# Optimization experiments

Measured on AMD Instinct MI355X. Metric: run time of the kernel, lower is better.

Reference implementation:

```python
import jax, jax.numpy as jnp
import numpy as np

B, N, D, H, F = 2, 2048, 512, 8, 8
HD = D // H

def setup_inputs() -> dict:
    key = jax.random.key(0)
    ks = jax.random.split(key, 11)
    s = 1.0 / np.sqrt(D)
    return {
        "x": jax.random.normal(ks[0], (B, N, D), dtype=jnp.float32),
        "phase_coords": jax.random.uniform(ks[1], (B, N, F), dtype=jnp.float32) * 6.28,
        "Wq": jax.random.normal(ks[2], (D, D), dtype=jnp.float32) * s,
        "bq": jax.random.normal(ks[3], (D,), dtype=jnp.float32) * 0.01,
        "Wk": jax.random.normal(ks[4], (D, D), dtype=jnp.float32) * s,
        "bk": jax.random.normal(ks[5], (D,), dtype=jnp.float32) * 0.01,
        "Wv": jax.random.normal(ks[6], (D, D), dtype=jnp.float32) * s,
        "bv": jax.random.normal(ks[7], (D,), dtype=jnp.float32) * 0.01,
        "Wo": jax.random.normal(ks[8], (D, D), dtype=jnp.float32) * s,
        "bo": jax.random.normal(ks[9], (D,), dtype=jnp.float32) * 0.01,
        "phase_bias": jax.random.normal(ks[10], (H, F), dtype=jnp.float32) * 0.1,
    }

def reference(x, phase_coords, Wq, bq, Wk, bk, Wv, bv, Wo, bo, phase_bias):
    b, n, _ = x.shape
    def proj(W, bias):
        # [B,N,D] -> [B,H,N,HD]
        return (x @ W.T + bias).reshape(b, n, H, HD).transpose(0, 2, 1, 3)
    Q, K, V = proj(Wq, bq), proj(Wk, bk), proj(Wv, bv)
    scores = jnp.einsum("bhqd,bhkd->bhqk", Q, K) / np.sqrt(HD)
    # phase coherence bias: cos of pairwise phase diffs, weighted per head
    phase_diff = phase_coords[:, :, None, :] - phase_coords[:, None, :, :]  # [B,N,N,F]
    coherence = jnp.cos(phase_diff)
    bias = jnp.einsum("bqkf,hf->bhqk", coherence, phase_bias)
    scores = scores + bias
    attn = jax.nn.softmax(scores, axis=-1)
    attended = jnp.einsum("bhqk,bhkd->bhqd", attn, V)
    attended = attended.transpose(0, 2, 1, 3).reshape(b, n, D)
    return attended @ Wo.T + bo
```

## Files before the change

### kernel.cpp

```cpp
#include <hip/hip_runtime.h>
#include <stdint.h>

typedef unsigned short u16;
typedef unsigned int   u32;
typedef __bf16 bf16x8 __attribute__((ext_vector_type(8)));
typedef float  f32x4  __attribute__((ext_vector_type(4)));
typedef u16    u16x8  __attribute__((ext_vector_type(8)));
typedef u16    u16x4  __attribute__((ext_vector_type(4)));

#define B_  2
#define N_  2048
#define D_  512
#define H_  8
#define HD_ 64

__device__ __forceinline__ u16 f2bf(float f) {
  union { float f; u32 u; } v; v.f = f;
  u32 r = v.u + 0x7FFFu + ((v.u >> 16) & 1u);
  return (u16)(r >> 16);
}
__device__ __forceinline__ float bf2f(u16 s) {
  union { u32 u; float f; } v; v.u = ((u32)s) << 16; return v.f;
}

__device__ __forceinline__ void gload_lds16(const void* g, void* l) {
  __builtin_amdgcn_global_load_lds(
      (const __attribute__((address_space(1))) void*)g,
      (__attribute__((address_space(3))) void*)l, 16, 0, 0);
}

__global__ __launch_bounds__(256) void k_prep(
    const float* __restrict__ x, const float* __restrict__ pc,
    const float* __restrict__ Wq, const float* __restrict__ bq,
    const float* __restrict__ Wk, const float* __restrict__ bk,
    const float* __restrict__ Wv, const float* __restrict__ bv,
    const float* __restrict__ Wo,
    u16* __restrict__ xb, u16* __restrict__ wqkvb, float* __restrict__ bqkv,
    u16* __restrict__ wob, u16* __restrict__ pcs)
{
  int gid = blockIdx.x * blockDim.x + threadIdx.x;
  int stride = gridDim.x * blockDim.x;
  for (int i = gid; i < B_ * N_ * D_; i += stride) xb[i] = f2bf(x[i]);
  for (int i = gid; i < 3 * D_ * D_; i += stride) {
    int r = i >> 9;
    float v;
    if (r < 512)       v = Wq[i] * 0.125f;
    else if (r < 1024) v = Wk[i - 512 * 512];
    else               v = Wv[i - 1024 * 512];
    wqkvb[i] = f2bf(v);
  }
  for (int i = gid; i < 3 * D_; i += stride) {
    float v;
    if (i < 512)       v = bq[i] * 0.125f;
    else if (i < 1024) v = bk[i - 512];
    else               v = bv[i - 1024];
    bqkv[i] = v;
  }
  for (int i = gid; i < D_ * D_; i += stride) wob[i] = f2bf(Wo[i]);
  for (int i = gid; i < B_ * N_; i += stride) {
#pragma unroll
    for (int f = 0; f < 8; f++) {
      float a = pc[i * 8 + f];
      pcs[i * 16 + f]     = f2bf(__cosf(a));
      pcs[i * 16 + 8 + f] = f2bf(__sinf(a));
    }
  }
}

template <int MODE>
__global__ __launch_bounds__(256) void k_gemm(
    const u16* __restrict__ A, const u16* __restrict__ Bm,
    const float* __restrict__ bias,
    u16* __restrict__ Qp, u16* __restrict__ Kp, u16* __restrict__ Vt,
    float* __restrict__ Of)
{
  __shared__ u16 As[2][64 * 64];
  __shared__ u16 Bs[2][128 * 64];
  const int tid = threadIdx.x;
  const int wave = tid >> 6, lane = tid & 63;
  const int fr = lane & 15, kg = lane >> 4;
  const int m0 = blockIdx.x * 64, n0 = blockIdx.y * 128;
  const int wr = (wave >> 1) * 32, wc = (wave & 1) * 64;

  f32x4 acc[2][4];
#pragma unroll
  for (int i = 0; i < 2; i++)
#pragma unroll
    for (int j = 0; j < 4; j++)
#pragma unroll
      for (int r = 0; r < 4; r++) acc[i][j][r] = 0.f;

  auto stage = [&](int buf, int k0) {
#pragma unroll
    for (int u = 0; u < 2; u++) {
      int chunk = (wave * 2 + u) * 64 + lane;
      int row = chunk >> 3, cl = chunk & 7;
      gload_lds16(A + (size_t)(m0 + row) * 512 + k0 + ((cl ^ (row & 7)) << 3),
                  &As[buf][(wave * 2 + u) * 512]);
    }
#pragma unroll
    for (int u = 0; u < 4; u++) {
      int chunk = (wave * 4 + u) * 64 + lane;
      int row = chunk >> 3, cl = chunk & 7;
      gload_lds16(Bm + (size_t)(n0 + row) * 512 + k0 + ((cl ^ (row & 7)) << 3),
                  &Bs[buf][(wave * 4 + u) * 512]);
    }
  };

  stage(0, 0);
  asm volatile("s_waitcnt vmcnt(0)" ::: "memory");
  __syncthreads();

#pragma unroll
  for (int s = 0; s < 8; s++) {
    const int cb = s & 1;
    if (s < 7) stage(cb ^ 1, (s + 1) * 64);
#pragma unroll
    for (int ksub = 0; ksub < 2; ksub++) {
      bf16x8 af[2], bf[4];
#pragma unroll
      for (int i = 0; i < 2; i++)
        af[i] = *(const bf16x8*)&As[cb][(wr + i * 16 + fr) * 64 + (((ksub * 4 + kg) ^ (fr & 7)) << 3)];
#pragma unroll
      for (int j = 0; j < 4; j++)
        bf[j] = *(const bf16x8*)&Bs[cb][(wc + j * 16 + fr) * 64 + (((ksub * 4 + kg) ^ (fr & 7)) << 3)];
#pragma unroll
      for (int i = 0; i < 2; i++)
#pragma unroll
        for (int j = 0; j < 4; j++)
          acc[i][j] = __builtin_amdgcn_mfma_f32_16x16x32_bf16(af[i], bf[j], acc[i][j], 0, 0, 0);
    }
    asm volatile("s_waitcnt vmcnt(0)" ::: "memory");
    __syncthreads();
  }

  if (MODE == 1) {
#pragma unroll
    for (int j = 0; j < 4; j++) {
      int col = n0 + wc + j * 16 + fr;
      float bc = bias[col];
#pragma unroll
      for (int i = 0; i < 2; i++)
#pragma unroll
        for (int r = 0; r < 4; r++)
          Of[(size_t)(m0 + wr + i * 16 + kg * 4 + r) * 512 + col] = acc[i][j][r] + bc;
  } } else {
    const int seg = n0 >> 9;
    const int nb = n0 & 511;
    if (seg < 2) {
      u16* dst = seg ? Kp : Qp;
#pragma unroll
      for (int j = 0; j < 4; j++) {
        int col = nb + wc + j * 16 + fr;
        float bc = bias[n0 + wc + j * 16 + fr];
#pragma unroll
        for (int i = 0; i < 2; i++)
#pragma unroll
          for (int r = 0; r < 4; r++)
            dst[(size_t)(m0 + wr + i * 16 + kg * 4 + r) * 512 + col] = f2bf(acc[i][j][r] + bc);
      }
    } else {
#pragma unroll
      for (int j = 0; j < 4; j++) {
        int cc = nb + wc + j * 16 + fr;
        float bc = bias[n0 + wc + j * 16 + fr];
        int h = cc >> 6, d = cc & 63;
#pragma unroll
        for (int i = 0; i < 2; i++) {
          int row = m0 + wr + i * 16 + kg * 4;
          int b = row >> 11, n = row & 2047;
          u16x4 o;
#pragma unroll
          for (int r = 0; r < 4; r++) o[r] = f2bf(acc[i][j][r] + bc);
          *(u16x4*)&Vt[((size_t)(b * 8 + h) * 64 + d) * N_ + n] = o;
        }
      }
    }
  }
}

__global__ __launch_bounds__(256) void k_attn(
    const u16* __restrict__ Qp, const u16* __restrict__ Kp,
    const u16* __restrict__ Vt, const u16* __restrict__ pcs,
    const float* __restrict__ pb, u16* __restrict__ att)
{
  const int bh = blockIdx.y, b = bh >> 3, h = bh & 7;
  const int q0 = blockIdx.x * 64;
  const int tid = threadIdx.x, wave = tid >> 6, lane = tid & 63;
  const int fr = lane & 15, kg = lane >> 4;

  __shared__ u16 Klds[2][64 * 72];
  __shared__ u16 Kext[2][64 * 40];
  __shared__ u16 Vlds[2][64 * 72];
  __shared__ u16 Plds[4][16 * 72];

  for (int i = tid; i < 2 * 64 * 16; i += 256) {
    int bb = i >> 10, rr = (i >> 4) & 63, c = 16 + (i & 15);
    Kext[bb][rr * 40 + c] = 0;
  }

  const int r0 = tid >> 3, c0 = (tid & 7) * 8;
  const int r1 = 32 + r0;
  const int er = tid >> 1, ec = (tid & 1) * 8;

  bf16x8 qa[3];
  {
    int gq = b * N_ + q0 + wave * 16 + fr;
#pragma unroll
    for (int ks = 0; ks < 2; ks++)
      qa[ks] = *(const bf16x8*)&Qp[(size_t)gq * D_ + h * HD_ + ks * 32 + kg * 8];
    union { bf16x8 v; u16 s[8]; } qe;
    if (kg < 2) {
      u16x8 cs = *(const u16x8*)&pcs[(size_t)gq * 16 + kg * 8];
#pragma unroll
      for (int j = 0; j < 8; j++) qe.s[j] = f2bf(pb[h * 8 + j] * bf2f(cs[j]));
    } else {
#pragma unroll
      for (int j = 0; j < 8; j++) qe.s[j] = 0;
    }
    qa[2] = qe.v;
  }

  f32x4 accO[4];
#pragma unroll
  for (int d = 0; d < 4; d++)
#pragma unroll
    for (int r = 0; r < 4; r++) accO[d][r] = 0.f;
  float Lacc[4] = {0.f, 0.f, 0.f, 0.f};

  {
    u16x8 k0v = *(const u16x8*)&Kp[(size_t)(b * N_ + r0) * D_ + h * HD_ + c0];
    u16x8 k1v = *(const u16x8*)&Kp[(size_t)(b * N_ + r1) * D_ + h * HD_ + c0];
    u16x8 v0v = *(const u16x8*)&Vt[((size_t)bh * HD_ + r0) * N_ + c0];
    u16x8 v1v = *(const u16x8*)&Vt[((size_t)bh * HD_ + r1) * N_ + c0];
    *(u16x8*)&Klds[0][r0 * 72 + c0] = k0v;
    *(u16x8*)&Klds[0][r1 * 72 + c0] = k1v;
    *(u16x8*)&Vlds[0][r0 * 72 + c0] = v0v;
    *(u16x8*)&Vlds[0][r1 * 72 + c0] = v1v;
    if (tid < 128) {
      u16x8 ev = *(const u16x8*)&pcs[(size_t)(b * N_ + er) * 16 + ec];
      *(u16x8*)&Kext[0][er * 40 + ec] = ev;
    }
  }
  __syncthreads();

  for (int t = 0; t < 32; t++) {
    const int cb = t & 1;
    const bool pf = (t < 31);
    u16x8 kreg0, kreg1, vreg0, vreg1, ereg;
    if (pf) {
      int nk = (t + 1) * 64;
      kreg0 = *(const u16x8*)&Kp[(size_t)(b * N_ + nk + r0) * D_ + h * HD_ + c0];
      kreg1 = *(const u16x8*)&Kp[(size_t)(b * N_ + nk + r1) * D_ + h * HD_ + c0];
      vreg0 = *(const u16x8*)&Vt[((size_t)bh * HD_ + r0) * N_ + nk + c0];
      vreg1 = *(const u16x8*)&Vt[((size_t)bh * HD_ + r1) * N_ + nk + c0];
      if (tid < 128) ereg = *(const u16x8*)&pcs[(size_t)(b * N_ + nk + er) * 16 + ec];
    }

    f32x4 accS[4];
#pragma unroll
    for (int j = 0; j < 4; j++)
#pragma unroll
      for (int r = 0; r < 4; r++) accS[j][r] = 0.f;
#pragma unroll
    for (int ks = 0; ks < 2; ks++) {
#pragma unroll
      for (int j = 0; j < 4; j++) {
        bf16x8 kb = *(const bf16x8*)&Klds[cb][(j * 16 + fr) * 72 + ks * 32 + kg * 8];
        accS[j] = __builtin_amdgcn_mfma_f32_16x16x32_bf16(qa[ks], kb, accS[j], 0, 0, 0);
      }
    }
#pragma unroll
    for (int j = 0; j < 4; j++) {
      bf16x8 kb = *(const bf16x8*)&Kext[cb][(j * 16 + fr) * 40 + kg * 8];
      accS[j] = __builtin_amdgcn_mfma_f32_16x16x32_bf16(qa[2], kb, accS[j], 0, 0, 0);
    }

#pragma unroll
    for (int j = 0; j < 4; j++) {
#pragma unroll
      for (int r = 0; r < 4; r++) {
        float p = __expf(accS[j][r] - 8.0f);
        Lacc[r] += p;
        Plds[wave][(kg * 4 + r) * 72 + j * 16 + fr] = f2bf(p);
      }
    }
    asm volatile("s_waitcnt lgkmcnt(0)" ::: "memory");
    __builtin_amdgcn_sched_barrier(0);

#pragma unroll
    for (int ks = 0; ks < 2; ks++) {
      bf16x8 pa = *(const bf16x8*)&Plds[wave][fr * 72 + ks * 32 + kg * 8];
#pragma unroll
      for (int d = 0; d < 4; d++) {
        bf16x8 vb = *(const bf16x8*)&Vlds[cb][(d * 16 + fr) * 72 + ks * 32 + kg * 8];
        accO[d] = __builtin_amdgcn_mfma_f32_16x16x32_bf16(pa, vb, accO[d], 0, 0, 0);
      }
    }

    if (pf) {
      *(u16x8*)&Klds[cb ^ 1][r0 * 72 + c0] = kreg0;
      *(u16x8*)&Klds[cb ^ 1][r1 * 72 + c0] = kreg1;
      *(u16x8*)&Vlds[cb ^ 1][r0 * 72 + c0] = vreg0;
      *(u16x8*)&Vlds[cb ^ 1][r1 * 72 + c0] = vreg1;
      if (tid < 128) *(u16x8*)&Kext[cb ^ 1][er * 40 + ec] = ereg;
    }
    __syncthreads();
  }

#pragma unroll
  for (int r = 0; r < 4; r++) {
    float l = Lacc[r];
    l += __shfl_xor(l, 1); l += __shfl_xor(l, 2);
    l += __shfl_xor(l, 4); l += __shfl_xor(l, 8);
    float inv = 1.0f / l;
    int q = q0 + wave * 16 + kg * 4 + r;
#pragma unroll
    for (int d = 0; d < 4; d++)
      att[(size_t)(b * N_ + q) * D_ + h * HD_ + d * 16 + fr] = f2bf(accO[d][r] * inv);
  }
}

extern "C" void kernel_launch(void* const* d_in, const int* in_sizes, int n_in,
                              void* d_out, int out_size, void* d_ws, size_t ws_size,
                              hipStream_t stream)
{
  (void)in_sizes; (void)n_in; (void)out_size; (void)ws_size;
  const float* x  = (const float*)d_in[0];
  const float* pc = (const float*)d_in[1];
  const float* Wq = (const float*)d_in[2];
  const float* bq = (const float*)d_in[3];
  const float* Wk = (const float*)d_in[4];
  const float* bk = (const float*)d_in[5];
  const float* Wv = (const float*)d_in[6];
  const float* bv = (const float*)d_in[7];
  const float* Wo = (const float*)d_in[8];
  const float* bo = (const float*)d_in[9];
  const float* pb = (const float*)d_in[10];

  u16* ws = (u16*)d_ws;
  const size_t TOK = (size_t)B_ * N_;
  u16* xb    = ws;
  u16* Qp    = xb    + TOK * D_;
  u16* Kp    = Qp    + TOK * D_;
  u16* Vt    = Kp    + TOK * D_;
  u16* attb  = Vt    + TOK * D_;
  u16* wqkvb = attb  + TOK * D_;
  u16* wob   = wqkvb + (size_t)3 * D_ * D_;
  u16* pcs   = wob   + (size_t)D_ * D_;
  float* bqkv = (float*)(pcs + TOK * 16);

  k_prep<<<1024, 256, 0, stream>>>(x, pc, Wq, bq, Wk, bk, Wv, bv, Wo,
                                   xb, wqkvb, bqkv, wob, pcs);
  k_gemm<0><<<dim3(64, 12), 256, 0, stream>>>(xb, wqkvb, bqkv, Qp, Kp, Vt, nullptr);
  k_attn<<<dim3(32, 16), 256, 0, stream>>>(Qp, Kp, Vt, pcs, pb, attb);
  k_gemm<1><<<dim3(64, 4), 256, 0, stream>>>(attb, wob, bo, nullptr, nullptr, nullptr, (float*)d_out);
}
```

Before: 150.3 us.

## Triple-buffer GEMM loads, shrink output-GEMM tile, use exp2 and swizzled P stores

The GEMM kernel moves from double to triple buffering with partial vmcnt waits, so two stages of loads are in flight and one barrier per step is dropped. The output projection gets a BN=64 tile, which doubles its grid to put more blocks on the GPU. In the attention kernel, log2(e) is folded into the Q scale and phase bias so softmax can call the native exp2 directly. P is now written with truncating bf16 conversion and an XOR swizzle to cut LDS bank conflicts. Risks are higher LDS use, which may lower occupancy, and slightly less precise P values from truncation.

```diff
diff --git a/kernel.cpp b/kernel.cpp
--- a/kernel.cpp
+++ b/kernel.cpp
@@ -19,6 +19,10 @@
   u32 r = v.u + 0x7FFFu + ((v.u >> 16) & 1u);
   return (u16)(r >> 16);
 }
+__device__ __forceinline__ u16 f2bf_trunc(float f) {
+  union { float f; u32 u; } v; v.f = f;
+  return (u16)(v.u >> 16);
+}
 __device__ __forceinline__ float bf2f(u16 s) {
   union { u32 u; float f; } v; v.u = ((u32)s) << 16; return v.f;
 }
@@ -28,6 +32,8 @@
       (const __attribute__((address_space(1))) void*)g,
       (__attribute__((address_space(3))) void*)l, 16, 0, 0);
 }
+
+#define LOG2E 1.4426950408889634f
 
 __global__ __launch_bounds__(256) void k_prep(
     const float* __restrict__ x, const float* __restrict__ pc,
@@ -40,18 +46,19 @@
 {
   int gid = blockIdx.x * blockDim.x + threadIdx.x;
   int stride = gridDim.x * blockDim.x;
+  const float qs = 0.125f * LOG2E;
   for (int i = gid; i < B_ * N_ * D_; i += stride) xb[i] = f2bf(x[i]);
   for (int i = gid; i < 3 * D_ * D_; i += stride) {
     int r = i >> 9;
     float v;
-    if (r < 512)       v = Wq[i] * 0.125f;
+    if (r < 512)       v = Wq[i] * qs;
     else if (r < 1024) v = Wk[i - 512 * 512];
     else               v = Wv[i - 1024 * 512];
     wqkvb[i] = f2bf(v);
   }
   for (int i = gid; i < 3 * D_; i += stride) {
     float v;
-    if (i < 512)       v = bq[i] * 0.125f;
+    if (i < 512)       v = bq[i] * qs;
     else if (i < 1024) v = bk[i - 512];
     else               v = bv[i - 1024];
     bqkv[i] = v;
@@ -67,26 +74,28 @@
   }
 }
 
-template <int MODE>
+template <int MODE, int BN>
 __global__ __launch_bounds__(256) void k_gemm(
     const u16* __restrict__ A, const u16* __restrict__ Bm,
     const float* __restrict__ bias,
     u16* __restrict__ Qp, u16* __restrict__ Kp, u16* __restrict__ Vt,
     float* __restrict__ Of)
 {
-  __shared__ u16 As[2][64 * 64];
-  __shared__ u16 Bs[2][128 * 64];
+  constexpr int JT  = BN / 32;
+  constexpr int BNC = BN / 32;
+  __shared__ u16 As[3][64 * 64];
+  __shared__ u16 Bs[3][BN * 64];
   const int tid = threadIdx.x;
   const int wave = tid >> 6, lane = tid & 63;
   const int fr = lane & 15, kg = lane >> 4;
-  const int m0 = blockIdx.x * 64, n0 = blockIdx.y * 128;
-  const int wr = (wave >> 1) * 32, wc = (wave & 1) * 64;
-
-  f32x4 acc[2][4];
+  const int m0 = blockIdx.x * 64, n0 = blockIdx.y * BN;
+  const int wr = (wave >> 1) * 32, wc = (wave & 1) * (BN / 2);
+
+  f32x4 acc[2][JT];
 #pragma unroll
   for (int i = 0; i < 2; i++)
 #pragma unroll
-    for (int j = 0; j < 4; j++)
+    for (int j = 0; j < JT; j++)
 #pragma unroll
       for (int r = 0; r < 4; r++) acc[i][j][r] = 0.f;
 
@@ -99,44 +108,48 @@
                   &As[buf][(wave * 2 + u) * 512]);
     }
 #pragma unroll
-    for (int u = 0; u < 4; u++) {
-      int chunk = (wave * 4 + u) * 64 + lane;
+    for (int u = 0; u < BNC; u++) {
+      int chunk = (wave * BNC + u) * 64 + lane;
       int row = chunk >> 3, cl = chunk & 7;
       gload_lds16(Bm + (size_t)(n0 + row) * 512 + k0 + ((cl ^ (row & 7)) << 3),
-                  &Bs[buf][(wave * 4 + u) * 512]);
+                  &Bs[buf][(wave * BNC + u) * 512]);
     }
   };
 
   stage(0, 0);
-  asm volatile("s_waitcnt vmcnt(0)" ::: "memory");
-  __syncthreads();
+  stage(1, 64);
 
 #pragma unroll
   for (int s = 0; s < 8; s++) {
-    const int cb = s & 1;
-    if (s < 7) stage(cb ^ 1, (s + 1) * 64);
+    if (s < 7) {
+      if constexpr (BN == 128) asm volatile("s_waitcnt vmcnt(6)" ::: "memory");
+      else                     asm volatile("s_waitcnt vmcnt(4)" ::: "memory");
+    } else {
+      asm volatile("s_waitcnt vmcnt(0)" ::: "memory");
+    }
+    __syncthreads();
+    if (s < 6) stage((s + 2) % 3, (s + 2) * 64);
+    const int cb = s % 3;
 #pragma unroll
     for (int ksub = 0; ksub < 2; ksub++) {
-      bf16x8 af[2], bf[4];
+      bf16x8 af[2], bf[JT];
 #pragma unroll
       for (int i = 0; i < 2; i++)
         af[i] = *(const bf16x8*)&As[cb][(wr + i * 16 + fr) * 64 + (((ksub * 4 + kg) ^ (fr & 7)) << 3)];
 #pragma unroll
-      for (int j = 0; j < 4; j++)
+      for (int j = 0; j < JT; j++)
         bf[j] = *(const bf16x8*)&Bs[cb][(wc + j * 16 + fr) * 64 + (((ksub * 4 + kg) ^ (fr & 7)) << 3)];
 #pragma unroll
       for (int i = 0; i < 2; i++)
 #pragma unroll
-        for (int j = 0; j < 4; j++)
+        for (int j = 0; j < JT; j++)
           acc[i][j] = __builtin_amdgcn_mfma_f32_16x16x32_bf16(af[i], bf[j], acc[i][j], 0, 0, 0);
     }
-    asm volatile("s_waitcnt vmcnt(0)" ::: "memory");
-    __syncthreads();
   }
 
   if (MODE == 1) {
 #pragma unroll
-    for (int j = 0; j < 4; j++) {
+    for (int j = 0; j < JT; j++) {
       int col = n0 + wc + j * 16 + fr;
       float bc = bias[col];
 #pragma unroll
@@ -150,7 +163,7 @@
     if (seg < 2) {
       u16* dst = seg ? Kp : Qp;
 #pragma unroll
-      for (int j = 0; j < 4; j++) {
+      for (int j = 0; j < JT; j++) {
         int col = nb + wc + j * 16 + fr;
         float bc = bias[n0 + wc + j * 16 + fr];
 #pragma unroll
@@ -161,7 +174,7 @@
       }
     } else {
 #pragma unroll
-      for (int j = 0; j < 4; j++) {
+      for (int j = 0; j < JT; j++) {
         int cc = nb + wc + j * 16 + fr;
         float bc = bias[n0 + wc + j * 16 + fr];
         int h = cc >> 6, d = cc & 63;
@@ -213,7 +226,7 @@
     if (kg < 2) {
       u16x8 cs = *(const u16x8*)&pcs[(size_t)gq * 16 + kg * 8];
 #pragma unroll
-      for (int j = 0; j < 8; j++) qe.s[j] = f2bf(pb[h * 8 + j] * bf2f(cs[j]));
+      for (int j = 0; j < 8; j++) qe.s[j] = f2bf(pb[h * 8 + j] * LOG2E * bf2f(cs[j]));
     } else {
 #pragma unroll
       for (int j = 0; j < 8; j++) qe.s[j] = 0;
@@ -280,9 +293,10 @@
     for (int j = 0; j < 4; j++) {
 #pragma unroll
       for (int r = 0; r < 4; r++) {
-        float p = __expf(accS[j][r] - 8.0f);
+        float p = __builtin_amdgcn_exp2f(accS[j][r] - 11.5415603f);
         Lacc[r] += p;
-        Plds[wave][(kg * 4 + r) * 72 + j * 16 + fr] = f2bf(p);
+        int rw = kg * 4 + r;
+        Plds[wave][rw * 72 + ((j * 16 + fr) ^ ((rw & 8) << 1))] = f2bf_trunc(p);
       }
     }
     asm volatile("s_waitcnt lgkmcnt(0)" ::: "memory");
@@ -290,7 +304,7 @@
 
 #pragma unroll
     for (int ks = 0; ks < 2; ks++) {
-      bf16x8 pa = *(const bf16x8*)&Plds[wave][fr * 72 + ks * 32 + kg * 8];
+      bf16x8 pa = *(const bf16x8*)&Plds[wave][fr * 72 + ((ks * 32 + kg * 8) ^ ((fr & 8) << 1))];
 #pragma unroll
       for (int d = 0; d < 4; d++) {
         bf16x8 vb = *(const bf16x8*)&Vlds[cb][(d * 16 + fr) * 72 + ks * 32 + kg * 8];
@@ -352,7 +366,7 @@
 
   k_prep<<<1024, 256, 0, stream>>>(x, pc, Wq, bq, Wk, bk, Wv, bv, Wo,
                                    xb, wqkvb, bqkv, wob, pcs);
-  k_gemm<0><<<dim3(64, 12), 256, 0, stream>>>(xb, wqkvb, bqkv, Qp, Kp, Vt, nullptr);
+  k_gemm<0, 128><<<dim3(64, 12), 256, 0, stream>>>(xb, wqkvb, bqkv, Qp, Kp, Vt, nullptr);
   k_attn<<<dim3(32, 16), 256, 0, stream>>>(Qp, Kp, Vt, pcs, pb, attb);
-  k_gemm<1><<<dim3(64, 4), 256, 0, stream>>>(attb, wob, bo, nullptr, nullptr, nullptr, (float*)d_out);
-}
+  k_gemm<1, 64><<<dim3(64, 8), 256, 0, stream>>>(attb, wob, bo, nullptr, nullptr, nullptr, (float*)d_out);
+}
```

New measurement: 152.9 us. No clear change (+1.7%).
